# Performance work log

Measured on AMD Instinct MI355X. Metric: run time of the kernel, lower is better.

The kernel has to match this reference:

```python
import jax, jax.numpy as jnp
import numpy as np

CH = 128

def _fir_kernel(ch, factor=2.0):
    # [1,3,3,1] outer product, normalized, scaled by factor**2 (== torch get_fir_kernel)
    k1 = jnp.array([1.0, 3.0, 3.0, 1.0], dtype=jnp.float32)
    k = jnp.outer(k1, k1)
    k = k / k.sum() * (factor ** 2)          # 4x4, sums to 4
    return jnp.tile(k[None, None], (ch, 1, 1, 1))  # (C,1,4,4) OIHW depthwise

def setup_inputs() -> dict:
    key = jax.random.key(0)
    x = jax.random.normal(key, (8, CH, 128, 128), dtype=jnp.float32)
    return {"x": x}

def reference(x) -> jnp.ndarray:
    B, C, H, W = x.shape
    k = _fir_kernel(C, factor=2.0)
    # torch F.conv_transpose2d(x, k, stride=2, padding=1, groups=C)
    # == forward conv with lhs_dilation=2, padding k-1-p=2 each side, spatially flipped kernel
    kf = k[:, :, ::-1, ::-1]  # symmetric kernel, flip for exactness
    out = jax.lax.conv_general_dilated(
        x, kf,
        window_strides=(1, 1),
        padding=((2, 2), (2, 2)),
        lhs_dilation=(2, 2),
        rhs_dilation=(1, 1),
        dimension_numbers=("NCHW", "OIHW", "NCHW"),
        feature_group_count=C,
    )
    # out shape: (B, C, 2H, 2W)
    return out
```

## Files before the change

### kernel.cpp

```cpp
#include <hip/hip_runtime.h>


#define IN_H 128
#define IN_W 128

__global__ __launch_bounds__(256) void upsample_fir_kernel(
    const float* __restrict__ x, float* __restrict__ out, int total) {
    int t = blockIdx.x * blockDim.x + threadIdx.x;
    if (t >= total) return;

    int ix = t & (IN_W - 1);
    int iy = (t >> 7) & (IN_H - 1);
    int bc = t >> 14;

    const float* xp = x + (size_t)bc * IN_H * IN_W;

    float v[3][3];
#pragma unroll
    for (int dy = -1; dy <= 1; ++dy) {
        int yy = iy + dy;
        bool yok = (unsigned)yy < IN_H;
#pragma unroll
        for (int dx = -1; dx <= 1; ++dx) {
            int xx = ix + dx;
            bool ok = yok && ((unsigned)xx < IN_W);
            v[dy + 1][dx + 1] = ok ? xp[yy * IN_W + xx] : 0.0f;
        }
    }

    float he[3], ho[3];
#pragma unroll
    for (int r = 0; r < 3; ++r) {
        he[r] = (v[r][0] + 3.0f * v[r][1]) * 0.25f;
        ho[r] = (3.0f * v[r][1] + v[r][2]) * 0.25f;
    }

    float2 top, bot;
    top.x = (he[0] + 3.0f * he[1]) * 0.25f;
    top.y = (ho[0] + 3.0f * ho[1]) * 0.25f;
    bot.x = (3.0f * he[1] + he[2]) * 0.25f;
    bot.y = (3.0f * ho[1] + ho[2]) * 0.25f;

    const int OW = 2 * IN_W;
    size_t ob = (size_t)bc * (2 * IN_H) * OW + (size_t)(2 * iy) * OW + 2 * ix;
    *(float2*)(out + ob) = top;
    *(float2*)(out + ob + OW) = bot;
}

extern "C" void kernel_launch(void* const* d_in, const int* in_sizes, int n_in,
                              void* d_out, int out_size, void* d_ws, size_t ws_size,
                              hipStream_t stream) {
    const float* x = (const float*)d_in[0];
    float* out = (float*)d_out;
    int total = in_sizes[0];
    int threads = 256;
    int blocks = (total + threads - 1) / threads;
    upsample_fir_kernel<<<blocks, threads, 0, stream>>>(x, out, total);
}
```

Baseline: 343.0 us.

## Process four pixels per thread with float4 loads and shuffle halos

Each 32-lane group now handles one full input row, loading float4 values from three rows and exchanging horizontal halo values with warp shuffles. Output is written as four float4 stores per thread. The goal is fewer, wider memory transactions and less redundant neighbour loading. In exchange, the input shape and the launch grid are hardcoded.

```diff
diff --git a/kernel.cpp b/kernel.cpp
--- a/kernel.cpp
+++ b/kernel.cpp
@@ -5,46 +5,60 @@
 #define IN_W 128
 
 __global__ __launch_bounds__(256) void upsample_fir_kernel(
-    const float* __restrict__ x, float* __restrict__ out, int total) {
-    int t = blockIdx.x * blockDim.x + threadIdx.x;
-    if (t >= total) return;
+    const float* __restrict__ x, float* __restrict__ out) {
+    const int tid = threadIdx.x;
+    const int lane32 = tid & 31;
+    const int r = blockIdx.x * 8 + (tid >> 5);
+    const int bc = r >> 7;
+    const int iy = r & (IN_H - 1);
 
-    int ix = t & (IN_W - 1);
-    int iy = (t >> 7) & (IN_H - 1);
-    int bc = t >> 14;
+    const float* xp = x + (size_t)bc * (IN_H * IN_W);
+    const float4 z4 = make_float4(0.f, 0.f, 0.f, 0.f);
 
-    const float* xp = x + (size_t)bc * IN_H * IN_W;
+    const float4* rowm = (const float4*)(xp + (iy - 1) * IN_W);
+    const float4* row0 = (const float4*)(xp + iy * IN_W);
+    const float4* rowp = (const float4*)(xp + (iy + 1) * IN_W);
 
-    float v[3][3];
-#pragma unroll
-    for (int dy = -1; dy <= 1; ++dy) {
-        int yy = iy + dy;
-        bool yok = (unsigned)yy < IN_H;
-#pragma unroll
-        for (int dx = -1; dx <= 1; ++dx) {
-            int xx = ix + dx;
-            bool ok = yok && ((unsigned)xx < IN_W);
-            v[dy + 1][dx + 1] = ok ? xp[yy * IN_W + xx] : 0.0f;
-        }
-    }
+    float4 a = (iy > 0) ? rowm[lane32] : z4;
+    float4 b = row0[lane32];
+    float4 c = (iy < IN_H - 1) ? rowp[lane32] : z4;
 
-    float he[3], ho[3];
-#pragma unroll
-    for (int r = 0; r < 3; ++r) {
-        he[r] = (v[r][0] + 3.0f * v[r][1]) * 0.25f;
-        ho[r] = (3.0f * v[r][1] + v[r][2]) * 0.25f;
-    }
+    float4 t, u;
+    t.x = (a.x + 3.f * b.x) * 0.25f;  u.x = (3.f * b.x + c.x) * 0.25f;
+    t.y = (a.y + 3.f * b.y) * 0.25f;  u.y = (3.f * b.y + c.y) * 0.25f;
+    t.z = (a.z + 3.f * b.z) * 0.25f;  u.z = (3.f * b.z + c.z) * 0.25f;
+    t.w = (a.w + 3.f * b.w) * 0.25f;  u.w = (3.f * b.w + c.w) * 0.25f;
 
-    float2 top, bot;
-    top.x = (he[0] + 3.0f * he[1]) * 0.25f;
-    top.y = (ho[0] + 3.0f * ho[1]) * 0.25f;
-    bot.x = (3.0f * he[1] + he[2]) * 0.25f;
-    bot.y = (3.0f * ho[1] + ho[2]) * 0.25f;
+    float t_l = __shfl_up(t.w, 1);   if (lane32 == 0)  t_l = 0.f;
+    float t_r = __shfl_down(t.x, 1); if (lane32 == 31) t_r = 0.f;
+    float u_l = __shfl_up(u.w, 1);   if (lane32 == 0)  u_l = 0.f;
+    float u_r = __shfl_down(u.x, 1); if (lane32 == 31) u_r = 0.f;
+
+    float4 o0, o1, p0, p1;
+    o0.x = (t_l + 3.f * t.x) * 0.25f;
+    o0.y = (3.f * t.x + t.y) * 0.25f;
+    o0.z = (t.x + 3.f * t.y) * 0.25f;
+    o0.w = (3.f * t.y + t.z) * 0.25f;
+    o1.x = (t.y + 3.f * t.z) * 0.25f;
+    o1.y = (3.f * t.z + t.w) * 0.25f;
+    o1.z = (t.z + 3.f * t.w) * 0.25f;
+    o1.w = (3.f * t.w + t_r) * 0.25f;
+
+    p0.x = (u_l + 3.f * u.x) * 0.25f;
+    p0.y = (3.f * u.x + u.y) * 0.25f;
+    p0.z = (u.x + 3.f * u.y) * 0.25f;
+    p0.w = (3.f * u.y + u.z) * 0.25f;
+    p1.x = (u.y + 3.f * u.z) * 0.25f;
+    p1.y = (3.f * u.z + u.w) * 0.25f;
+    p1.z = (u.z + 3.f * u.w) * 0.25f;
+    p1.w = (3.f * u.w + u_r) * 0.25f;
 
     const int OW = 2 * IN_W;
-    size_t ob = (size_t)bc * (2 * IN_H) * OW + (size_t)(2 * iy) * OW + 2 * ix;
-    *(float2*)(out + ob) = top;
-    *(float2*)(out + ob + OW) = bot;
+    float* ob = out + (size_t)bc * (2 * IN_H) * OW + (size_t)(2 * iy) * OW + 8 * lane32;
+    *(float4*)(ob) = o0;
+    *(float4*)(ob + 4) = o1;
+    *(float4*)(ob + OW) = p0;
+    *(float4*)(ob + OW + 4) = p1;
 }
 
 extern "C" void kernel_launch(void* const* d_in, const int* in_sizes, int n_in,
@@ -52,8 +66,6 @@
                               hipStream_t stream) {
     const float* x = (const float*)d_in[0];
     float* out = (float*)d_out;
-    int total = in_sizes[0];
-    int threads = 256;
-    int blocks = (total + threads - 1) / threads;
-    upsample_fir_kernel<<<blocks, threads, 0, stream>>>(x, out, total);
+    int blocks = (8 * 128 * 128) / 8;
+    upsample_fir_kernel<<<blocks, 256, 0, stream>>>(x, out);
 }
```

Result: faster. 334.4 us (-2.5%).
